# Performance work log

Measured on AMD Instinct MI355X. Metric: run time of the kernel, lower is better.

Reference implementation:

```python
import jax, jax.numpy as jnp
import numpy as np

B, I, O, H = 1024, 64, 64, 32  # batch, input_size, output_size, hidden_size
NEG_SLOPE = 0.01  # nn.LeakyReLU default


def leaky(x):
    return jnp.where(x >= 0, x, NEG_SLOPE * x)


def setup_inputs() -> dict:
    key = jax.random.key(0)
    ks = jax.random.split(key, 9)
    u = lambda k, shape, b: jax.random.uniform(k, shape, jnp.float32, -b, b)
    # Per-edge tiny MLP params, stacked over [O, I] edges.
    # Linear(1,H): fan_in=1 -> bound 1.0 ; Linear(H,H)/Linear(H,1): bound 1/sqrt(H)
    bnd = 1.0 / np.sqrt(H)
    return {
        "x": jax.random.normal(ks[0], (B, I), jnp.float32),
        "W1": u(ks[1], (O, I, H), 1.0),        # Linear(1,H) weight
        "b1": u(ks[2], (O, I, H), 1.0),
        "W2": u(ks[3], (O, I, H, H), bnd),     # Linear(H,H) weight [out,in]
        "b2": u(ks[4], (O, I, H), bnd),
        "W3": u(ks[5], (O, I, H), bnd),        # Linear(H,1) weight
        "b3": u(ks[6], (O, I), bnd),
        "layer_w": jnp.ones((O, I), jnp.float32),           # layer_weight init 1.0
        "bias_w": u(ks[7], (O, I), 0.1),                     # bias_weight ~ U(-0.1,0.1)
    }


def reference(x, W1, b1, W2, b2, W3, b3, layer_w, bias_w):
    # All O*I edge MLPs evaluated as one batched computation.
    # h1[b,o,i,h] = leaky(x[b,i] * W1[o,i,h] + b1[o,i,h])
    h1 = leaky(x[:, None, :, None] * W1 + b1)                      # [B,O,I,H]
    h2 = leaky(jnp.einsum('boih,oikh->boik', h1, W2) + b2)         # [B,O,I,H]
    edge = jnp.einsum('boih,oih->boi', h2, W3) + b3                # [B,O,I]
    edge = bias_w * leaky(x)[:, None, :] + layer_w * edge          # per-edge output
    return edge.sum(axis=2)                                        # [B,O]
```

## Files before the change

### kernel.cpp

```cpp
#include <hip/hip_runtime.h>


#define H_   32
#define NI   64
#define NO   64
#define NB   1024
#define ROWS 64
#define XSTR 66
#define NWAVE 8

typedef float    floatx4 __attribute__((ext_vector_type(4)));
typedef _Float16 halfx8  __attribute__((ext_vector_type(8)));
typedef _Float16 halfx2  __attribute__((ext_vector_type(2)));

union H8 { halfx8 v8; halfx2 v2[4]; unsigned int u[4]; };

__device__ inline float leaky(float v) { return fmaxf(v, 0.01f * v); }

__device__ inline unsigned int pkrtz(float a, float b) {
    return __builtin_bit_cast(unsigned int, __builtin_amdgcn_cvt_pkrtz(a, b));
}

__global__ __launch_bounds__(512, 6)
void kan_kernel(const float* __restrict__ x,  const float* __restrict__ W1,
                const float* __restrict__ b1, const float* __restrict__ W2,
                const float* __restrict__ b2, const float* __restrict__ W3,
                const float* __restrict__ b3, const float* __restrict__ lw,
                const float* __restrict__ bw, float* __restrict__ out)
{
    __shared__ unsigned int xsp[ROWS * XSTR];
    __shared__ _Float16 w1s[NI * H_];
    __shared__ _Float16 b1s[NI * H_];
    __shared__ unsigned int wbs[NI * H_];
    __shared__ float rc[ROWS];
    __shared__ float part[NWAVE][ROWS];

    const int t    = threadIdx.x;
    const int o    = blockIdx.x;
    const int row0 = blockIdx.y * ROWS;

    const float* xsrc = x + (size_t)row0 * NI;
    #pragma unroll
    for (int v = 0; v < 2; ++v) {
        int fe = (v * 512 + t) * 4;
        int r = fe >> 6, c = fe & 63;
        float4 xv = *(const float4*)(xsrc + fe);
        uint2 lo = { pkrtz(xv.x, xv.x), pkrtz(xv.y, xv.y) };
        uint2 hi = { pkrtz(xv.z, xv.z), pkrtz(xv.w, xv.w) };
        *(uint2*)(&xsp[r * XSTR + c])     = lo;
        *(uint2*)(&xsp[r * XSTR + c + 2]) = hi;
    }
    const float* w1g = W1 + (size_t)o * NI * H_;
    const float* b1g = b1 + (size_t)o * NI * H_;
    {
        int e = t * 4;
        float4 a = *(const float4*)(w1g + e);
        float4 c = *(const float4*)(b1g + e);
        uint2 pa = { pkrtz(a.x, a.y), pkrtz(a.z, a.w) };
        uint2 pc = { pkrtz(c.x, c.y), pkrtz(c.z, c.w) };
        *(uint2*)(w1s + e) = pa;
        *(uint2*)(b1s + e) = pc;
    }
    {
        int e = t * 4;
        float l = lw[o * NI + (e >> 5)];
        const float* w3g = W3 + (size_t)o * NI * H_ + e;
        const float* b2g = b2 + (size_t)o * NI * H_ + e;
        float4 wa = *(const float4*)(w3g);
        float4 ba = *(const float4*)(b2g);
        uint4 p0 = { pkrtz(l * wa.x, ba.x), pkrtz(l * wa.y, ba.y),
                     pkrtz(l * wa.z, ba.z), pkrtz(l * wa.w, ba.w) };
        *(uint4*)(&wbs[e]) = p0;
    }
    __syncthreads();

    if (t < ROWS) {
        float s = 0.f;
        const float* bwp = bw + o * NI;
        const float* lp  = lw + o * NI;
        const float* b3p = b3 + o * NI;
        for (int i = 0; i < NI; ++i) {
            halfx2 hx = __builtin_bit_cast(halfx2, xsp[t * XSTR + i]);
            s += bwp[i] * leaky((float)hx[0]) + lp[i] * b3p[i];
        }
        rc[t] = s;
    }

    const int lane = t & 63, wave = t >> 6;
    const int col  = lane & 15;
    const int kh   = lane >> 4;
    const int koff = kh * 8;
    const int i0   = wave * 8;

    const float* w2p0 = W2 + ((size_t)(o * NI + i0) * H_ + col) * H_ + koff;
    const float* w2p1 = w2p0 + 16 * H_;
    const halfx2 slope = { (_Float16)0.01f, (_Float16)0.01f };

    floatx4 pacc[4] = { {0,0,0,0}, {0,0,0,0}, {0,0,0,0}, {0,0,0,0} };

    #pragma unroll 2
    for (int ii = 0; ii < 8; ++ii) {
        const int i = i0 + ii;

        floatx4 a0 = *(const floatx4*)(w2p0);
        floatx4 a1 = *(const floatx4*)(w2p0 + 4);
        floatx4 a2 = *(const floatx4*)(w2p1);
        floatx4 a3 = *(const floatx4*)(w2p1 + 4);
        H8 bf0, bf1;
        bf0.u[0] = pkrtz(a0[0], a0[1]);  bf0.u[1] = pkrtz(a0[2], a0[3]);
        bf0.u[2] = pkrtz(a1[0], a1[1]);  bf0.u[3] = pkrtz(a1[2], a1[3]);
        bf1.u[0] = pkrtz(a2[0], a2[1]);  bf1.u[1] = pkrtz(a2[2], a2[3]);
        bf1.u[2] = pkrtz(a3[0], a3[1]);  bf1.u[3] = pkrtz(a3[2], a3[3]);

        H8 w1v, b1v;
        w1v.v8 = *(const halfx8*)(w1s + i * H_ + koff);
        b1v.v8 = *(const halfx8*)(b1s + i * H_ + koff);

        halfx2 q0 = __builtin_bit_cast(halfx2, wbs[i * H_ + col]);
        halfx2 q1 = __builtin_bit_cast(halfx2, wbs[i * H_ + col + 16]);
        float w3e0 = (float)q0[0], b2c0 = (float)q0[1];
        float w3e1 = (float)q1[0], b2c1 = (float)q1[1];
        float p0 = 0.505f * w3e0, n0 = 0.495f * w3e0;
        float p1 = 0.505f * w3e1, n1 = 0.495f * w3e1;

        #pragma unroll
        for (int m = 0; m < 4; ++m) {
            halfx2 xx = __builtin_bit_cast(halfx2, xsp[(m * 16 + col) * XSTR + i]);
            H8 af;
            #pragma unroll
            for (int j = 0; j < 4; ++j) {
                halfx2 h = __builtin_elementwise_fma(xx, w1v.v2[j], b1v.v2[j]);
                af.v2[j] = __builtin_elementwise_max(h, h * slope);
            }
            floatx4 c0 = { b2c0, b2c0, b2c0, b2c0 };
            floatx4 c1 = { b2c1, b2c1, b2c1, b2c1 };
            c0 = __builtin_amdgcn_mfma_f32_16x16x32_f16(af.v8, bf0.v8, c0, 0, 0, 0);
            c1 = __builtin_amdgcn_mfma_f32_16x16x32_f16(af.v8, bf1.v8, c1, 0, 0, 0);
            #pragma unroll
            for (int r = 0; r < 4; ++r) {
                pacc[m][r] = fmaf(p0, c0[r],
                             fmaf(n0, fabsf(c0[r]),
                             fmaf(p1, c1[r],
                             fmaf(n1, fabsf(c1[r]), pacc[m][r]))));
            }
        }

        w2p0 += H_ * H_;  w2p1 += H_ * H_;
    }

    #pragma unroll
    for (int m = 0; m < 4; ++m) {
        #pragma unroll
        for (int r = 0; r < 4; ++r) {
            float v = pacc[m][r];
            v += __shfl_xor(v, 1, 64);
            v += __shfl_xor(v, 2, 64);
            v += __shfl_xor(v, 4, 64);
            v += __shfl_xor(v, 8, 64);
            if (col == 0)
                part[wave][m * 16 + kh * 4 + r] = v;
        }
    }
    __syncthreads();

    if (t < ROWS) {
        float v = rc[t];
        #pragma unroll
        for (int w = 0; w < NWAVE; ++w) v += part[w][t];
        out[(size_t)(row0 + t) * NO + o] = v;
    }
}

extern "C" void kernel_launch(void* const* d_in, const int* in_sizes, int n_in,
                              void* d_out, int out_size, void* d_ws, size_t ws_size,
                              hipStream_t stream) {
    const float* x  = (const float*)d_in[0];
    const float* W1 = (const float*)d_in[1];
    const float* b1 = (const float*)d_in[2];
    const float* W2 = (const float*)d_in[3];
    const float* b2 = (const float*)d_in[4];
    const float* W3 = (const float*)d_in[5];
    const float* b3 = (const float*)d_in[6];
    const float* lw = (const float*)d_in[7];
    const float* bw = (const float*)d_in[8];
    float* out = (float*)d_out;

    dim3 grid(NO, NB / ROWS);
    kan_kernel<<<grid, dim3(512), 0, stream>>>(x, W1, b1, W2, b2, W3, b3, lw, bw, out);
}
```

Measured before the change: 115.4 us.

## Double rows per block and prefetch next W2 slice in registers

```diff
diff --git a/kernel.cpp b/kernel.cpp
--- a/kernel.cpp
+++ b/kernel.cpp
@@ -5,7 +5,8 @@
 #define NI   64
 #define NO   64
 #define NB   1024
-#define ROWS 64
+#define ROWS 128
+#define MT   8
 #define XSTR 66
 #define NWAVE 8
 
@@ -21,7 +22,7 @@
     return __builtin_bit_cast(unsigned int, __builtin_amdgcn_cvt_pkrtz(a, b));
 }
 
-__global__ __launch_bounds__(512, 6)
+__global__ __launch_bounds__(512, 4)
 void kan_kernel(const float* __restrict__ x,  const float* __restrict__ W1,
                 const float* __restrict__ b1, const float* __restrict__ W2,
                 const float* __restrict__ b2, const float* __restrict__ W3,
@@ -41,7 +42,7 @@
 
     const float* xsrc = x + (size_t)row0 * NI;
     #pragma unroll
-    for (int v = 0; v < 2; ++v) {
+    for (int v = 0; v < 4; ++v) {
         int fe = (v * 512 + t) * 4;
         int r = fe >> 6, c = fe & 63;
         float4 xv = *(const float4*)(xsrc + fe);
@@ -96,16 +97,30 @@
     const float* w2p1 = w2p0 + 16 * H_;
     const halfx2 slope = { (_Float16)0.01f, (_Float16)0.01f };
 
-    floatx4 pacc[4] = { {0,0,0,0}, {0,0,0,0}, {0,0,0,0}, {0,0,0,0} };
+    floatx4 pacc[MT];
+    #pragma unroll
+    for (int m = 0; m < MT; ++m)
+        pacc[m] = floatx4{0.f, 0.f, 0.f, 0.f};
+
+    floatx4 a0 = *(const floatx4*)(w2p0);
+    floatx4 a1 = *(const floatx4*)(w2p0 + 4);
+    floatx4 a2 = *(const floatx4*)(w2p1);
+    floatx4 a3 = *(const floatx4*)(w2p1 + 4);
 
     #pragma unroll 2
     for (int ii = 0; ii < 8; ++ii) {
         const int i = i0 + ii;
 
-        floatx4 a0 = *(const floatx4*)(w2p0);
-        floatx4 a1 = *(const floatx4*)(w2p0 + 4);
-        floatx4 a2 = *(const floatx4*)(w2p1);
-        floatx4 a3 = *(const floatx4*)(w2p1 + 4);
+        floatx4 n0, n1, n2, n3;
+        if (ii < 7) {
+            const float* np0 = w2p0 + (ii + 1) * (H_ * H_);
+            const float* np1 = w2p1 + (ii + 1) * (H_ * H_);
+            n0 = *(const floatx4*)(np0);
+            n1 = *(const floatx4*)(np0 + 4);
+            n2 = *(const floatx4*)(np1);
+            n3 = *(const floatx4*)(np1 + 4);
+        }
+
         H8 bf0, bf1;
         bf0.u[0] = pkrtz(a0[0], a0[1]);  bf0.u[1] = pkrtz(a0[2], a0[3]);
         bf0.u[2] = pkrtz(a1[0], a1[1]);  bf0.u[3] = pkrtz(a1[2], a1[3]);
@@ -120,11 +135,11 @@
         halfx2 q1 = __builtin_bit_cast(halfx2, wbs[i * H_ + col + 16]);
         float w3e0 = (float)q0[0], b2c0 = (float)q0[1];
         float w3e1 = (float)q1[0], b2c1 = (float)q1[1];
-        float p0 = 0.505f * w3e0, n0 = 0.495f * w3e0;
-        float p1 = 0.505f * w3e1, n1 = 0.495f * w3e1;
+        float p0 = 0.505f * w3e0, nn0 = 0.495f * w3e0;
+        float p1 = 0.505f * w3e1, nn1 = 0.495f * w3e1;
 
         #pragma unroll
-        for (int m = 0; m < 4; ++m) {
+        for (int m = 0; m < MT; ++m) {
             halfx2 xx = __builtin_bit_cast(halfx2, xsp[(m * 16 + col) * XSTR + i]);
             H8 af;
             #pragma unroll
@@ -138,18 +153,20 @@
             c1 = __builtin_amdgcn_mfma_f32_16x16x32_f16(af.v8, bf1.v8, c1, 0, 0, 0);
             #pragma unroll
             for (int r = 0; r < 4; ++r) {
-                pacc[m][r] = fmaf(p0, c0[r],
-                             fmaf(n0, fabsf(c0[r]),
-                             fmaf(p1, c1[r],
-                             fmaf(n1, fabsf(c1[r]), pacc[m][r]))));
+                float acc = pacc[m][r];
+                acc = fmaf(p0,  c0[r],
+                      fmaf(nn0, fabsf(c0[r]),
+                      fmaf(p1,  c1[r],
+                      fmaf(nn1, fabsf(c1[r]), acc))));
+                pacc[m][r] = acc;
             }
         }
 
-        w2p0 += H_ * H_;  w2p1 += H_ * H_;
+        a0 = n0; a1 = n1; a2 = n2; a3 = n3;
     }
 
     #pragma unroll
-    for (int m = 0; m < 4; ++m) {
+    for (int m = 0; m < MT; ++m) {
         #pragma unroll
         for (int r = 0; r < 4; ++r) {
             float v = pacc[m][r];
```

Result: no change. 114.6 us (-0.7%).
